# Kernel tuning notes

Hardware: AMD Instinct MI355X
Metric: run time of the kernel (lower is better)

Reference implementation:

```python
import jax, jax.numpy as jnp
import numpy as np

EMBED_DIM = 64  # matches init_kwargs embed_dim; used for 1/sqrt(d) scaling


def setup_inputs() -> dict:
    key = jax.random.key(0)
    k1, k2, k3, k4 = jax.random.split(key, 4)
    N1, N2, C, B = 8192, 8192, EMBED_DIM, 8
    query = jax.random.normal(k1, (N1, C), dtype=jnp.float32)
    key_value = jax.random.normal(k2, (N2, C), dtype=jnp.float32)
    # sorted batch indices so per-batch concat order == input row order
    query_coors = jnp.sort(jax.random.randint(k3, (N1,), 0, B))
    key_value_coors = jnp.sort(jax.random.randint(k4, (N2,), 0, B))
    return {
        "query": query,
        "key_value": key_value,
        "query_coors": query_coors,
        "key_value_coors": key_value_coors,
    }


def reference(query, key_value, query_coors, key_value_coors):
    # Per-batch attention: each query row attends only to key_value rows with
    # the same batch index. Equivalent to the original per-batch loop +
    # chunked softmax(QK^T/sqrt(d)) V, expressed as one masked attention.
    # Dropout is identity (eval mode) for a deterministic correctness baseline.
    scale = 1.0 / jnp.sqrt(jnp.asarray(EMBED_DIM, dtype=query.dtype))
    scores = jnp.einsum("nc,mc->nm", query, key_value) * scale  # [N1, N2]
    same_batch = query_coors[:, None] == key_value_coors[None, :]
    neg_inf = jnp.asarray(-jnp.inf, dtype=scores.dtype)
    scores = jnp.where(same_batch, scores, neg_inf)
    attn = jax.nn.softmax(scores, axis=-1)  # softmax within each batch segment
    out = jnp.einsum("nm,mc->nc", attn, key_value)  # [N1, C]
    return out
```

## Files before the change

kernel.cpp:

```cpp
#include <hip/hip_runtime.h>
#include <hip/hip_bf16.h>

typedef __attribute__((ext_vector_type(8))) short bf16x8;
typedef __attribute__((ext_vector_type(8))) unsigned short u16x8;
typedef __attribute__((ext_vector_type(4))) float f32x4;

#define NEG_INF (-__builtin_inff())
#define SPLIT 4

static __device__ __forceinline__ unsigned short f2bf(float x) {
  union { float f; unsigned u; } v; v.f = x;
  unsigned r = (v.u + 0x7fffu + ((v.u >> 16) & 1u)) >> 16;
  return (unsigned short)r;
}

__global__ void prep_kv_kernel(const float* __restrict__ kv, const int* __restrict__ kvc,
                               unsigned short* __restrict__ kvb, unsigned short* __restrict__ kvt,
                               int* __restrict__ seg, int nkv) {
  __shared__ unsigned short tile[32][64];
  const int kv0 = blockIdx.x * 32;
  const int t = threadIdx.x;
  if (t < 32) {
    int i = kv0 + t;
    if (i < nkv) {
      int c = kvc[i];
      int cp = (i == 0) ? -1 : kvc[i - 1];
      if (c != cp) {
        for (int b = cp + 1; b <= c; ++b) seg[b] = i;
        if (i == 0) for (int b = 0; b < c; ++b) seg[8 + b] = 0;
      }
      int cn = (i == nkv - 1) ? 8 : kvc[i + 1];
      if (c != cn) {
        for (int b = c; b < cn; ++b) seg[8 + b] = i + 1;
        if (i == nkv - 1) for (int b = c + 1; b < 8; ++b) seg[b] = nkv;
      }
    }
  }
  int r = (t * 8) >> 6;
  int c = (t * 8) & 63;
  const float4* src = (const float4*)(kv + (size_t)(kv0 + r) * 64 + c);
  float4 a = src[0], b = src[1];
  u16x8 v;
  v[0] = f2bf(a.x); v[1] = f2bf(a.y); v[2] = f2bf(a.z); v[3] = f2bf(a.w);
  v[4] = f2bf(b.x); v[5] = f2bf(b.y); v[6] = f2bf(b.z); v[7] = f2bf(b.w);
  *(u16x8*)&tile[r][c] = v;
  *(u16x8*)(kvb + (size_t)(kv0 + r) * 64 + c) = v;
  __syncthreads();
  int d = t & 63;
  int k0 = (t >> 6) * 8;
  u16x8 w;
#pragma unroll
  for (int j = 0; j < 8; ++j) w[j] = tile[k0 + j][d];
  *(u16x8*)(kvt + (size_t)blockIdx.x * 2048 + d * 32 + k0) = w;
}

#define LOADK(P, kvx)                                                          \
  {                                                                            \
    const unsigned short* kb_ = kvb + (((size_t)((kvx) + rowoff)) << 6) + g8;  \
    k##P##0 = *(const bf16x8*)(kb_);                                           \
    k##P##1 = *(const bf16x8*)(kb_ + 32);                                      \
    k##P##2 = *(const bf16x8*)(kb_ + 256);                                     \
    k##P##3 = *(const bf16x8*)(kb_ + 256 + 32);                                \
  }

#define COMPUTE(P, kvx)                                                        \
  {                                                                            \
    const int kv0_ = (kvx);                                                    \
    const unsigned short* vb_ = kvt + (((size_t)kv0_ >> 5) << 11) + q16 * 32 + g8; \
    bf16x8 vf0_ = *(const bf16x8*)(vb_);                                       \
    bf16x8 vf1_ = *(const bf16x8*)(vb_ + 512);                                 \
    bf16x8 vf2_ = *(const bf16x8*)(vb_ + 1024);                                \
    bf16x8 vf3_ = *(const bf16x8*)(vb_ + 1536);                                \
    f32x4 z_ = {0, 0, 0, 0};                                                   \
    __builtin_amdgcn_s_setprio(1);                                             \
    f32x4 sT0 = __builtin_amdgcn_mfma_f32_16x16x32_bf16(k##P##0, qf0, z_, 0, 0, 0); \
    sT0 = __builtin_amdgcn_mfma_f32_16x16x32_bf16(k##P##1, qf1, sT0, 0, 0, 0); \
    f32x4 sT1 = __builtin_amdgcn_mfma_f32_16x16x32_bf16(k##P##2, qf0, z_, 0, 0, 0); \
    sT1 = __builtin_amdgcn_mfma_f32_16x16x32_bf16(k##P##3, qf1, sT1, 0, 0, 0); \
    __builtin_amdgcn_s_setprio(0);                                             \
    float v_[8];                                                               \
    const bool full_ = uniformb && (kv0_ >= kv_lo) && (kv0_ + 32 <= kv_hi);    \
    if (full_) {                                                               \
      _Pragma("unroll") for (int r = 0; r < 4; ++r) {                          \
        v_[r] = sT0[r];                                                        \
        v_[4 + r] = sT1[r];                                                    \
      }                                                                        \
    } else {                                                                   \
      const int k0_ = kv0_ + g8;                                               \
      _Pragma("unroll") for (int r = 0; r < 4; ++r) {                          \
        v_[r]     = (k0_ + r     >= lo_q && k0_ + r     < hi_q) ? sT0[r] : NEG_INF; \
        v_[4 + r] = (k0_ + r + 4 >= lo_q && k0_ + r + 4 < hi_q) ? sT1[r] : NEG_INF; \
      }                                                                        \
    }                                                                          \
    float t_ = fmaxf(fmaxf(fmaxf(v_[0], v_[1]), fmaxf(v_[2], v_[3])),          \
                     fmaxf(fmaxf(v_[4], v_[5]), fmaxf(v_[6], v_[7])));         \
    t_ = fmaxf(t_, __shfl_xor(t_, 16));                                        \
    t_ = fmaxf(t_, __shfl_xor(t_, 32));                                        \
    float mn_ = fmaxf(m, t_);                                                  \
    float f_ = (mn_ == NEG_INF) ? 1.0f : __expf(m - mn_);                      \
    float e_[8];                                                               \
    _Pragma("unroll") for (int i = 0; i < 8; ++i)                              \
        e_[i] = (v_[i] == NEG_INF) ? 0.0f : __expf(v_[i] - mn_);               \
    l = l * f_ + (((e_[0] + e_[1]) + (e_[2] + e_[3])) +                        \
                  ((e_[4] + e_[5]) + (e_[6] + e_[7])));                        \
    m = mn_;                                                                   \
    _Pragma("unroll") for (int r = 0; r < 4; ++r) {                            \
      acc0[r] *= f_; acc1[r] *= f_; acc2[r] *= f_; acc3[r] *= f_;              \
    }                                                                          \
    bf16x8 pa_;                                                                \
    _Pragma("unroll") for (int j = 0; j < 8; ++j) pa_[j] = (short)f2bf(e_[j]); \
    __builtin_amdgcn_s_setprio(1);                                             \
    acc0 = __builtin_amdgcn_mfma_f32_16x16x32_bf16(vf0_, pa_, acc0, 0, 0, 0);  \
    acc1 = __builtin_amdgcn_mfma_f32_16x16x32_bf16(vf1_, pa_, acc1, 0, 0, 0);  \
    acc2 = __builtin_amdgcn_mfma_f32_16x16x32_bf16(vf2_, pa_, acc2, 0, 0, 0);  \
    acc3 = __builtin_amdgcn_mfma_f32_16x16x32_bf16(vf3_, pa_, acc3, 0, 0, 0);  \
    __builtin_amdgcn_s_setprio(0);                                             \
  }

__global__ __launch_bounds__(256, 4) void attn_kernel(
    const float* __restrict__ qf,
    const unsigned short* __restrict__ kvb,
    const unsigned short* __restrict__ kvt,
    const int* __restrict__ qc,
    const int* __restrict__ seg,
    float* __restrict__ out, int n2)
{
  __shared__ float macc[SPLIT][16][68];
  __shared__ float mml[SPLIT][16];
  __shared__ float mll[SPLIT][16];

  const int q0 = blockIdx.x * 16;
  const int w = threadIdx.x >> 6;
  const int lane = threadIdx.x & 63;
  const int q16 = lane & 15;
  const int g = lane >> 4;
  const int g8 = g * 8;

  const int myb = qc[q0 + q16];
  const int lo_q = seg[myb];
  const int hi_q = seg[8 + myb];
  const int bfirst = __shfl(myb, 0);
  const int blast  = __shfl(myb, 15);
  const int kv_lo  = __shfl(lo_q, 0);
  const int kv_hi  = __shfl(hi_q, 15);
  const bool uniformb = (bfirst == blast);

  bf16x8 qf0, qf1;
  {
    const float* qrow = qf + (size_t)(q0 + q16) * 64 + g8;
    float4 x0 = *(const float4*)(qrow);
    float4 x1 = *(const float4*)(qrow + 4);
    float4 x2 = *(const float4*)(qrow + 32);
    float4 x3 = *(const float4*)(qrow + 36);
    qf0[0]=(short)f2bf(x0.x*0.125f); qf0[1]=(short)f2bf(x0.y*0.125f);
    qf0[2]=(short)f2bf(x0.z*0.125f); qf0[3]=(short)f2bf(x0.w*0.125f);
    qf0[4]=(short)f2bf(x1.x*0.125f); qf0[5]=(short)f2bf(x1.y*0.125f);
    qf0[6]=(short)f2bf(x1.z*0.125f); qf0[7]=(short)f2bf(x1.w*0.125f);
    qf1[0]=(short)f2bf(x2.x*0.125f); qf1[1]=(short)f2bf(x2.y*0.125f);
    qf1[2]=(short)f2bf(x2.z*0.125f); qf1[3]=(short)f2bf(x2.w*0.125f);
    qf1[4]=(short)f2bf(x3.x*0.125f); qf1[5]=(short)f2bf(x3.y*0.125f);
    qf1[6]=(short)f2bf(x3.z*0.125f); qf1[7]=(short)f2bf(x3.w*0.125f);
  }

  const int base = kv_lo & ~31;
  const int nblk = (kv_hi - base + 31) >> 5;
  const int b0 = (nblk * w) / SPLIT;
  const int b1 = (nblk * (w + 1)) / SPLIT;

  const int rowoff = ((q16 >> 2) << 3) + (q16 & 3);

  f32x4 acc0 = {0,0,0,0}, acc1 = {0,0,0,0}, acc2 = {0,0,0,0}, acc3 = {0,0,0,0};
  float m = NEG_INF;
  float l = 0.0f;

  bf16x8 kA0, kA1, kA2, kA3, kB0, kB1, kB2, kB3;
  int b = b0;
  if (b < b1) {
    LOADK(A, base + b * 32);
    while (true) {
      if (b + 1 < b1) LOADK(B, base + (b + 1) * 32);
      COMPUTE(A, base + b * 32);
      ++b; if (b >= b1) break;
      if (b + 1 < b1) LOADK(A, base + (b + 1) * 32);
      COMPUTE(B, base + b * 32);
      ++b; if (b >= b1) break;
    }
  }

  l += __shfl_xor(l, 16);
  l += __shfl_xor(l, 32);

#pragma unroll
  for (int r = 0; r < 4; ++r) {
    macc[w][q16][0  + g * 4 + r] = acc0[r];
    macc[w][q16][16 + g * 4 + r] = acc1[r];
    macc[w][q16][32 + g * 4 + r] = acc2[r];
    macc[w][q16][48 + g * 4 + r] = acc3[r];
  }
  if (g == 0) { mml[w][q16] = m; mll[w][q16] = l; }
  __syncthreads();

  {
    const int t = threadIdx.x;
    const int i = t >> 4;
    const int c0 = (t & 15) * 4;
    float mstar = NEG_INF;
#pragma unroll
    for (int ww = 0; ww < SPLIT; ++ww) mstar = fmaxf(mstar, mml[ww][i]);
    float s[SPLIT];
    float L = 0.0f;
#pragma unroll
    for (int ww = 0; ww < SPLIT; ++ww) {
      float mw = mml[ww][i];
      s[ww] = (mw == NEG_INF) ? 0.0f : __expf(mw - mstar);
      L += s[ww] * mll[ww][i];
    }
    float inv = (L > 0.0f) ? 1.0f / L : 0.0f;
    f32x4 num = {0, 0, 0, 0};
#pragma unroll
    for (int ww = 0; ww < SPLIT; ++ww) {
      f32x4 a = *(const f32x4*)&macc[ww][i][c0];
      num[0] += s[ww] * a[0]; num[1] += s[ww] * a[1];
      num[2] += s[ww] * a[2]; num[3] += s[ww] * a[3];
    }
    float* o = out + (size_t)(q0 + i) * 64 + c0;
    o[0] = num[0] * inv; o[1] = num[1] * inv;
    o[2] = num[2] * inv; o[3] = num[3] * inv;
  }
}

extern "C" void kernel_launch(void* const* d_in, const int* in_sizes, int n_in,
                              void* d_out, int out_size, void* d_ws, size_t ws_size,
                              hipStream_t stream) {
  const float* q  = (const float*)d_in[0];
  const float* kv = (const float*)d_in[1];
  const int* qc   = (const int*)d_in[2];
  const int* kvc  = (const int*)d_in[3];
  float* out = (float*)d_out;

  const int C = 64;
  const int n1 = in_sizes[0] / C;
  const int n2 = in_sizes[1] / C;

  char* ws = (char*)d_ws;
  size_t off = 0;
  unsigned short* kvb = (unsigned short*)(ws + off); off += (size_t)n2 * C * 2;
  unsigned short* kvt = (unsigned short*)(ws + off); off += (size_t)n2 * C * 2;
  int* seg = (int*)(ws + off);

  prep_kv_kernel<<<n2 / 32, 256, 0, stream>>>(kv, kvc, kvb, kvt, seg, n2);
  attn_kernel<<<n1 / 16, 256, 0, stream>>>(q, kvb, kvt, qc, seg, out, n2);
}
```

Baseline: 30.40 us.

## Fuse KV prep into attention kernel via grid barrier; use exp2 with folded log2e

Merges the KV bf16 conversion, transpose and segment-boundary computation into the attention kernel. Each block converts 16 KV rows, then all blocks wait on an atomic grid-wide barrier, which removes a separate kernel launch. The query scale now folds in log2(e), so the softmax can use exp2 instead of exp. The spin barrier assumes all 512 blocks are resident at once, adds a memset, and could deadlock if occupancy is lower.

```diff
diff --git a/kernel.cpp b/kernel.cpp
--- a/kernel.cpp
+++ b/kernel.cpp
@@ -2,56 +2,17 @@
 #include <hip/hip_bf16.h>
 
 typedef __attribute__((ext_vector_type(8))) short bf16x8;
-typedef __attribute__((ext_vector_type(8))) unsigned short u16x8;
+typedef __attribute__((ext_vector_type(4))) unsigned short u16x4;
 typedef __attribute__((ext_vector_type(4))) float f32x4;
 
 #define NEG_INF (-__builtin_inff())
 #define SPLIT 4
+#define QSCALE (0.125f * 1.4426950408889634f)
 
 static __device__ __forceinline__ unsigned short f2bf(float x) {
   union { float f; unsigned u; } v; v.f = x;
   unsigned r = (v.u + 0x7fffu + ((v.u >> 16) & 1u)) >> 16;
   return (unsigned short)r;
-}
-
-__global__ void prep_kv_kernel(const float* __restrict__ kv, const int* __restrict__ kvc,
-                               unsigned short* __restrict__ kvb, unsigned short* __restrict__ kvt,
-                               int* __restrict__ seg, int nkv) {
-  __shared__ unsigned short tile[32][64];
-  const int kv0 = blockIdx.x * 32;
-  const int t = threadIdx.x;
-  if (t < 32) {
-    int i = kv0 + t;
-    if (i < nkv) {
-      int c = kvc[i];
-      int cp = (i == 0) ? -1 : kvc[i - 1];
-      if (c != cp) {
-        for (int b = cp + 1; b <= c; ++b) seg[b] = i;
-        if (i == 0) for (int b = 0; b < c; ++b) seg[8 + b] = 0;
-      }
-      int cn = (i == nkv - 1) ? 8 : kvc[i + 1];
-      if (c != cn) {
-        for (int b = c; b < cn; ++b) seg[8 + b] = i + 1;
-        if (i == nkv - 1) for (int b = c + 1; b < 8; ++b) seg[b] = nkv;
-      }
-    }
-  }
-  int r = (t * 8) >> 6;
-  int c = (t * 8) & 63;
-  const float4* src = (const float4*)(kv + (size_t)(kv0 + r) * 64 + c);
-  float4 a = src[0], b = src[1];
-  u16x8 v;
-  v[0] = f2bf(a.x); v[1] = f2bf(a.y); v[2] = f2bf(a.z); v[3] = f2bf(a.w);
-  v[4] = f2bf(b.x); v[5] = f2bf(b.y); v[6] = f2bf(b.z); v[7] = f2bf(b.w);
-  *(u16x8*)&tile[r][c] = v;
-  *(u16x8*)(kvb + (size_t)(kv0 + r) * 64 + c) = v;
-  __syncthreads();
-  int d = t & 63;
-  int k0 = (t >> 6) * 8;
-  u16x8 w;
-#pragma unroll
-  for (int j = 0; j < 8; ++j) w[j] = tile[k0 + j][d];
-  *(u16x8*)(kvt + (size_t)blockIdx.x * 2048 + d * 32 + k0) = w;
 }
 
 #define LOADK(P, kvx)                                                          \
@@ -97,10 +58,10 @@
     t_ = fmaxf(t_, __shfl_xor(t_, 16));                                        \
     t_ = fmaxf(t_, __shfl_xor(t_, 32));                                        \
     float mn_ = fmaxf(m, t_);                                                  \
-    float f_ = (mn_ == NEG_INF) ? 1.0f : __expf(m - mn_);                      \
+    float f_ = (mn_ == NEG_INF) ? 1.0f : __builtin_exp2f(m - mn_);             \
     float e_[8];                                                               \
     _Pragma("unroll") for (int i = 0; i < 8; ++i)                              \
-        e_[i] = (v_[i] == NEG_INF) ? 0.0f : __expf(v_[i] - mn_);               \
+        e_[i] = (v_[i] == NEG_INF) ? 0.0f : __builtin_exp2f(v_[i] - mn_);      \
     l = l * f_ + (((e_[0] + e_[1]) + (e_[2] + e_[3])) +                        \
                   ((e_[4] + e_[5]) + (e_[6] + e_[7])));                        \
     m = mn_;                                                                   \
@@ -117,50 +78,98 @@
     __builtin_amdgcn_s_setprio(0);                                             \
   }
 
-__global__ __launch_bounds__(256, 4) void attn_kernel(
+__global__ __launch_bounds__(256, 4) void fused_kernel(
     const float* __restrict__ qf,
-    const unsigned short* __restrict__ kvb,
-    const unsigned short* __restrict__ kvt,
+    const float* __restrict__ kv,
     const int* __restrict__ qc,
-    const int* __restrict__ seg,
+    const int* __restrict__ kvc,
+    unsigned short* __restrict__ kvb,
+    unsigned short* __restrict__ kvt,
+    int* __restrict__ seg,
+    unsigned* __restrict__ bar,
     float* __restrict__ out, int n2)
 {
+  __shared__ unsigned short tile[16][64];
   __shared__ float macc[SPLIT][16][68];
   __shared__ float mml[SPLIT][16];
   __shared__ float mll[SPLIT][16];
 
   const int q0 = blockIdx.x * 16;
-  const int w = threadIdx.x >> 6;
-  const int lane = threadIdx.x & 63;
+  const int tid = threadIdx.x;
+  const int w = tid >> 6;
+  const int lane = tid & 63;
   const int q16 = lane & 15;
   const int g = lane >> 4;
   const int g8 = g * 8;
-
+  const unsigned nblk_grid = gridDim.x;
+
+  const float* qrow = qf + (size_t)(q0 + q16) * 64 + g8;
+  float4 x0 = *(const float4*)(qrow);
+  float4 x1 = *(const float4*)(qrow + 4);
+  float4 x2 = *(const float4*)(qrow + 32);
+  float4 x3 = *(const float4*)(qrow + 36);
   const int myb = qc[q0 + q16];
+  const int bfirst = __shfl(myb, 0);
+  const int blast  = __shfl(myb, 15);
+  const bool uniformb = (bfirst == blast);
+
+  {
+    const int rowbase = blockIdx.x * 16;
+    if (tid < 16) {
+      int i = rowbase + tid;
+      int c = kvc[i];
+      int cp = (i == 0) ? -1 : kvc[i - 1];
+      if (c != cp) {
+        for (int b = cp + 1; b <= c; ++b) seg[b] = i;
+        if (i == 0) for (int b = 0; b < c; ++b) seg[8 + b] = 0;
+      }
+      int cn = (i == n2 - 1) ? 8 : kvc[i + 1];
+      if (c != cn) {
+        for (int b = c; b < cn; ++b) seg[8 + b] = i + 1;
+        if (i == n2 - 1) for (int b = c + 1; b < 8; ++b) seg[b] = n2;
+      }
+    }
+    const int r = tid >> 4;
+    const int c = (tid & 15) * 4;
+    float4 a = *(const float4*)(kv + (size_t)(rowbase + r) * 64 + c);
+    u16x4 v4;
+    v4[0] = f2bf(a.x); v4[1] = f2bf(a.y); v4[2] = f2bf(a.z); v4[3] = f2bf(a.w);
+    *(u16x4*)(kvb + (size_t)(rowbase + r) * 64 + c) = v4;
+    *(u16x4*)&tile[r][c] = v4;
+    __syncthreads();
+    const int d = tid & 63;
+    const int k0 = (tid >> 6) * 4;
+    u16x4 wv;
+#pragma unroll
+    for (int j = 0; j < 4; ++j) wv[j] = tile[k0 + j][d];
+    const int blk = rowbase >> 5;
+    const int kbase = (rowbase & 31) + k0;
+    *(u16x4*)(kvt + (size_t)blk * 2048 + d * 32 + kbase) = wv;
+  }
+
+  __syncthreads();
+  if (tid == 0) {
+    __threadfence();
+    __hip_atomic_fetch_add(bar, 1u, __ATOMIC_ACQ_REL, __HIP_MEMORY_SCOPE_AGENT);
+    while (__hip_atomic_load(bar, __ATOMIC_ACQUIRE, __HIP_MEMORY_SCOPE_AGENT) < nblk_grid)
+      __builtin_amdgcn_s_sleep(2);
+  }
+  __syncthreads();
+
+  bf16x8 qf0, qf1;
+  qf0[0]=(short)f2bf(x0.x*QSCALE); qf0[1]=(short)f2bf(x0.y*QSCALE);
+  qf0[2]=(short)f2bf(x0.z*QSCALE); qf0[3]=(short)f2bf(x0.w*QSCALE);
+  qf0[4]=(short)f2bf(x1.x*QSCALE); qf0[5]=(short)f2bf(x1.y*QSCALE);
+  qf0[6]=(short)f2bf(x1.z*QSCALE); qf0[7]=(short)f2bf(x1.w*QSCALE);
+  qf1[0]=(short)f2bf(x2.x*QSCALE); qf1[1]=(short)f2bf(x2.y*QSCALE);
+  qf1[2]=(short)f2bf(x2.z*QSCALE); qf1[3]=(short)f2bf(x2.w*QSCALE);
+  qf1[4]=(short)f2bf(x3.x*QSCALE); qf1[5]=(short)f2bf(x3.y*QSCALE);
+  qf1[6]=(short)f2bf(x3.z*QSCALE); qf1[7]=(short)f2bf(x3.w*QSCALE);
+
   const int lo_q = seg[myb];
   const int hi_q = seg[8 + myb];
-  const int bfirst = __shfl(myb, 0);
-  const int blast  = __shfl(myb, 15);
-  const int kv_lo  = __shfl(lo_q, 0);
-  const int kv_hi  = __shfl(hi_q, 15);
-  const bool uniformb = (bfirst == blast);
-
-  bf16x8 qf0, qf1;
-  {
-    const float* qrow = qf + (size_t)(q0 + q16) * 64 + g8;
-    float4 x0 = *(const float4*)(qrow);
-    float4 x1 = *(const float4*)(qrow + 4);
-    float4 x2 = *(const float4*)(qrow + 32);
-    float4 x3 = *(const float4*)(qrow + 36);
-    qf0[0]=(short)f2bf(x0.x*0.125f); qf0[1]=(short)f2bf(x0.y*0.125f);
-    qf0[2]=(short)f2bf(x0.z*0.125f); qf0[3]=(short)f2bf(x0.w*0.125f);
-    qf0[4]=(short)f2bf(x1.x*0.125f); qf0[5]=(short)f2bf(x1.y*0.125f);
-    qf0[6]=(short)f2bf(x1.z*0.125f); qf0[7]=(short)f2bf(x1.w*0.125f);
-    qf1[0]=(short)f2bf(x2.x*0.125f); qf1[1]=(short)f2bf(x2.y*0.125f);
-    qf1[2]=(short)f2bf(x2.z*0.125f); qf1[3]=(short)f2bf(x2.w*0.125f);
-    qf1[4]=(short)f2bf(x3.x*0.125f); qf1[5]=(short)f2bf(x3.y*0.125f);
-    qf1[6]=(short)f2bf(x3.z*0.125f); qf1[7]=(short)f2bf(x3.w*0.125f);
-  }
+  const int kv_lo = __shfl(lo_q, 0);
+  const int kv_hi = __shfl(hi_q, 15);
 
   const int base = kv_lo & ~31;
   const int nblk = (kv_hi - base + 31) >> 5;
@@ -212,7 +221,7 @@
 #pragma unroll
     for (int ww = 0; ww < SPLIT; ++ww) {
       float mw = mml[ww][i];
-      s[ww] = (mw == NEG_INF) ? 0.0f : __expf(mw - mstar);
+      s[ww] = (mw == NEG_INF) ? 0.0f : __builtin_exp2f(mw - mstar);
       L += s[ww] * mll[ww][i];
     }
     float inv = (L > 0.0f) ? 1.0f / L : 0.0f;
@@ -246,8 +255,9 @@
   size_t off = 0;
   unsigned short* kvb = (unsigned short*)(ws + off); off += (size_t)n2 * C * 2;
   unsigned short* kvt = (unsigned short*)(ws + off); off += (size_t)n2 * C * 2;
-  int* seg = (int*)(ws + off);
-
-  prep_kv_kernel<<<n2 / 32, 256, 0, stream>>>(kv, kvc, kvb, kvt, seg, n2);
-  attn_kernel<<<n1 / 16, 256, 0, stream>>>(q, kvb, kvt, qc, seg, out, n2);
+  int* seg = (int*)(ws + off); off += 64;
+  unsigned* bar = (unsigned*)(ws + off);
+
+  hipMemsetAsync(bar, 0, sizeof(unsigned), stream);
+  fused_kernel<<<n1 / 16, 256, 0, stream>>>(q, kv, qc, kvc, kvb, kvt, seg, bar, out, n2);
 }
```

Result: slower. 80.04 us (+163.3%).

## Use lazy softmax rescaling with exp2 and split KV across 8 waves

Applied to the files above, without the earlier changes.

Folds log2(e) into the query scale so the softmax uses exp2. It starts the running max at a fixed constant and skips the max reduction and accumulator rescale unless some lane exceeds the current max. It also doubles the KV split to 8 waves per block (512 threads) and adapts the cross-wave combine. This cuts per-tile shuffles, exps and multiplies and adds parallelism. The cost is more LDS for merging, and the numerics rely on scores staying below the fixed threshold unless a rescale is triggered.

```diff
diff --git a/kernel.cpp b/kernel.cpp
--- a/kernel.cpp
+++ b/kernel.cpp
@@ -6,7 +6,9 @@
 typedef __attribute__((ext_vector_type(4))) float f32x4;
 
 #define NEG_INF (-__builtin_inff())
-#define SPLIT 4
+#define SPLIT 8
+#define QSCALE (0.125f * 1.4426950408889634f)
+#define CONST_M 12.0f
 
 static __device__ __forceinline__ unsigned short f2bf(float x) {
   union { float f; unsigned u; } v; v.f = x;
@@ -92,21 +94,25 @@
         v_[4 + r] = (k0_ + r + 4 >= lo_q && k0_ + r + 4 < hi_q) ? sT1[r] : NEG_INF; \
       }                                                                        \
     }                                                                          \
+         \
     float t_ = fmaxf(fmaxf(fmaxf(v_[0], v_[1]), fmaxf(v_[2], v_[3])),          \
                      fmaxf(fmaxf(v_[4], v_[5]), fmaxf(v_[6], v_[7])));         \
-    t_ = fmaxf(t_, __shfl_xor(t_, 16));                                        \
-    t_ = fmaxf(t_, __shfl_xor(t_, 32));                                        \
-    float mn_ = fmaxf(m, t_);                                                  \
-    float f_ = (mn_ == NEG_INF) ? 1.0f : __expf(m - mn_);                      \
+    if (__builtin_expect(__any(t_ > m), 0)) {                                  \
+      float tt_ = fmaxf(t_, __shfl_xor(t_, 16));                               \
+      tt_ = fmaxf(tt_, __shfl_xor(tt_, 32));                                   \
+      float mn_ = fmaxf(m, tt_);                                               \
+      float f_ = __builtin_exp2f(m - mn_);                                     \
+      l *= f_;                                                                 \
+      _Pragma("unroll") for (int r = 0; r < 4; ++r) {                          \
+        acc0[r] *= f_; acc1[r] *= f_; acc2[r] *= f_; acc3[r] *= f_;            \
+      }                                                                        \
+      m = mn_;                                                                 \
+    }                                                                          \
     float e_[8];                                                               \
     _Pragma("unroll") for (int i = 0; i < 8; ++i)                              \
-        e_[i] = (v_[i] == NEG_INF) ? 0.0f : __expf(v_[i] - mn_);               \
-    l = l * f_ + (((e_[0] + e_[1]) + (e_[2] + e_[3])) +                        \
-                  ((e_[4] + e_[5]) + (e_[6] + e_[7])));                        \
-    m = mn_;                                                                   \
-    _Pragma("unroll") for (int r = 0; r < 4; ++r) {                            \
-      acc0[r] *= f_; acc1[r] *= f_; acc2[r] *= f_; acc3[r] *= f_;              \
-    }                                                                          \
+      e_[i] = __builtin_exp2f(v_[i] - m);          \
+    l += (((e_[0] + e_[1]) + (e_[2] + e_[3])) +                                \
+          ((e_[4] + e_[5]) + (e_[6] + e_[7])));                                \
     bf16x8 pa_;                                                                \
     _Pragma("unroll") for (int j = 0; j < 8; ++j) pa_[j] = (short)f2bf(e_[j]); \
     __builtin_amdgcn_s_setprio(1);                                             \
@@ -117,7 +123,7 @@
     __builtin_amdgcn_s_setprio(0);                                             \
   }
 
-__global__ __launch_bounds__(256, 4) void attn_kernel(
+__global__ __launch_bounds__(512, 4) void attn_kernel(
     const float* __restrict__ qf,
     const unsigned short* __restrict__ kvb,
     const unsigned short* __restrict__ kvt,
@@ -152,14 +158,14 @@
     float4 x1 = *(const float4*)(qrow + 4);
     float4 x2 = *(const float4*)(qrow + 32);
     float4 x3 = *(const float4*)(qrow + 36);
-    qf0[0]=(short)f2bf(x0.x*0.125f); qf0[1]=(short)f2bf(x0.y*0.125f);
-    qf0[2]=(short)f2bf(x0.z*0.125f); qf0[3]=(short)f2bf(x0.w*0.125f);
-    qf0[4]=(short)f2bf(x1.x*0.125f); qf0[5]=(short)f2bf(x1.y*0.125f);
-    qf0[6]=(short)f2bf(x1.z*0.125f); qf0[7]=(short)f2bf(x1.w*0.125f);
-    qf1[0]=(short)f2bf(x2.x*0.125f); qf1[1]=(short)f2bf(x2.y*0.125f);
-    qf1[2]=(short)f2bf(x2.z*0.125f); qf1[3]=(short)f2bf(x2.w*0.125f);
-    qf1[4]=(short)f2bf(x3.x*0.125f); qf1[5]=(short)f2bf(x3.y*0.125f);
-    qf1[6]=(short)f2bf(x3.z*0.125f); qf1[7]=(short)f2bf(x3.w*0.125f);
+    qf0[0]=(short)f2bf(x0.x*QSCALE); qf0[1]=(short)f2bf(x0.y*QSCALE);
+    qf0[2]=(short)f2bf(x0.z*QSCALE); qf0[3]=(short)f2bf(x0.w*QSCALE);
+    qf0[4]=(short)f2bf(x1.x*QSCALE); qf0[5]=(short)f2bf(x1.y*QSCALE);
+    qf0[6]=(short)f2bf(x1.z*QSCALE); qf0[7]=(short)f2bf(x1.w*QSCALE);
+    qf1[0]=(short)f2bf(x2.x*QSCALE); qf1[1]=(short)f2bf(x2.y*QSCALE);
+    qf1[2]=(short)f2bf(x2.z*QSCALE); qf1[3]=(short)f2bf(x2.w*QSCALE);
+    qf1[4]=(short)f2bf(x3.x*QSCALE); qf1[5]=(short)f2bf(x3.y*QSCALE);
+    qf1[6]=(short)f2bf(x3.z*QSCALE); qf1[7]=(short)f2bf(x3.w*QSCALE);
   }
 
   const int base = kv_lo & ~31;
@@ -170,7 +176,7 @@
   const int rowoff = ((q16 >> 2) << 3) + (q16 & 3);
 
   f32x4 acc0 = {0,0,0,0}, acc1 = {0,0,0,0}, acc2 = {0,0,0,0}, acc3 = {0,0,0,0};
-  float m = NEG_INF;
+  float m = CONST_M;
   float l = 0.0f;
 
   bf16x8 kA0, kA1, kA2, kA3, kB0, kB1, kB2, kB3;
@@ -202,8 +208,8 @@
 
   {
     const int t = threadIdx.x;
-    const int i = t >> 4;
-    const int c0 = (t & 15) * 4;
+    const int i = t >> 5;
+    const int c0 = (t & 31) * 2;
     float mstar = NEG_INF;
 #pragma unroll
     for (int ww = 0; ww < SPLIT; ++ww) mstar = fmaxf(mstar, mml[ww][i]);
@@ -212,20 +218,19 @@
 #pragma unroll
     for (int ww = 0; ww < SPLIT; ++ww) {
       float mw = mml[ww][i];
-      s[ww] = (mw == NEG_INF) ? 0.0f : __expf(mw - mstar);
+      s[ww] = __builtin_exp2f(mw - mstar);
       L += s[ww] * mll[ww][i];
     }
     float inv = (L > 0.0f) ? 1.0f / L : 0.0f;
-    f32x4 num = {0, 0, 0, 0};
+    float n0 = 0.0f, n1 = 0.0f;
 #pragma unroll
     for (int ww = 0; ww < SPLIT; ++ww) {
-      f32x4 a = *(const f32x4*)&macc[ww][i][c0];
-      num[0] += s[ww] * a[0]; num[1] += s[ww] * a[1];
-      num[2] += s[ww] * a[2]; num[3] += s[ww] * a[3];
+      n0 += s[ww] * macc[ww][i][c0];
+      n1 += s[ww] * macc[ww][i][c0 + 1];
     }
     float* o = out + (size_t)(q0 + i) * 64 + c0;
-    o[0] = num[0] * inv; o[1] = num[1] * inv;
-    o[2] = num[2] * inv; o[3] = num[3] * inv;
+    o[0] = n0 * inv;
+    o[1] = n1 * inv;
   }
 }
 
@@ -249,5 +254,5 @@
   int* seg = (int*)(ws + off);
 
   prep_kv_kernel<<<n2 / 32, 256, 0, stream>>>(kv, kvc, kvb, kvt, seg, n2);
-  attn_kernel<<<n1 / 16, 256, 0, stream>>>(q, kvb, kvt, qc, seg, out, n2);
-}
+  attn_kernel<<<n1 / 16, 512, 0, stream>>>(q, kvb, kvt, qc, seg, out, n2);
+}
```

New measurement: 31.38 us. +3.2%, slower.
